# Performance work log

Measured on AMD Instinct MI355X. Metric: run time of the kernel, lower is better.

## Reference

```python
import jax, jax.numpy as jnp
import numpy as np

N, H, S, D = 2, 8, 2048, 64

def setup_inputs() -> dict:
    key = jax.random.key(0)
    k1, k2, k3, k4 = jax.random.split(key, 4)
    queries = jax.random.normal(k1, (N, H, S, D), dtype=jnp.float32)
    keys = jax.random.normal(k2, (N, H, S, D), dtype=jnp.float32)
    values = jax.random.normal(k3, (N, H, S, D), dtype=jnp.float32)
    attn_mask = jax.random.randint(k4, (1, 1, S, S), 0, 2, dtype=jnp.int32)
    return {"queries": queries, "keys": keys, "values": values, "attn_mask": attn_mask}

def reference(queries, keys, values, attn_mask):
    # Faithful to the torch code: softmax over axis=2 (query/seq axis) for Q,
    # softmax over axis=1 (heads axis) for K, exactly as written.
    Q = jax.nn.softmax(queries, axis=2)
    K = jax.nn.softmax(keys, axis=1)
    attention_weights = jnp.einsum('nhqd,nhkd->nhqk', Q, K)  # [N,H,S,S]
    attention_weights = jnp.where(attn_mask == 0, -jnp.inf, attention_weights)
    attention_weights = jax.nn.softmax(attention_weights, axis=-1)
    context = jnp.einsum('nhqk,nhkd->nhqd', attention_weights, values)
    return context, attention_weights
```

## Files before the change

### kernel.cpp

```cpp
#include <hip/hip_runtime.h>

#define S 2048
#define Dh 64
#define NH 16
#define SD (S*Dh)
#define SSZ ((size_t)S*(size_t)S)

typedef __attribute__((ext_vector_type(4))) float f32x4;
typedef __attribute__((ext_vector_type(8))) short s16x8;

#define WSB_QSUM 0
#define WSB_RINV 4096
#define WSB_MASK 135168
#define WSB_QS   659456
#define WSB_KS   (WSB_QS + 4194304)
#define WSB_VT   (WSB_KS + 4194304)

__device__ __forceinline__ ushort f2bf(float x) {
    unsigned u = __builtin_bit_cast(unsigned, x);
    u = (u + 0x7fffu + ((u >> 16) & 1u)) >> 16;
    return (ushort)u;
}

__device__ __forceinline__ void gload_lds16(const ushort* g, ushort* l) {
    __builtin_amdgcn_global_load_lds(
        (const __attribute__((address_space(1))) unsigned int*)(const void*)g,
        (__attribute__((address_space(3))) unsigned int*)(void*)l,
        16, 0, 0);
}

__global__ void k_qsum(const float* __restrict__ q, float* __restrict__ qsum) {
    const int head  = blockIdx.x >> 5;
    const int chunk = blockIdx.x & 31;
    const int t = threadIdx.x;
    const int d = t & 63, sg = t >> 6;
    const float* qh = q + (size_t)head * SD;
    const int s0 = chunk * 64;
    float acc = 0.f;
#pragma unroll
    for (int i = 0; i < 16; ++i) {
        int s = s0 + sg + 4 * i;
        acc += __expf(qh[s * Dh + d]);
    }
    __shared__ float part[4][64];
    part[sg][d] = acc;
    __syncthreads();
    if (sg == 0)
        atomicAdd(&qsum[head * 64 + d], part[0][d] + part[1][d] + part[2][d] + part[3][d]);
}

__global__ void k_qnorm(const float* __restrict__ q, const float* __restrict__ qsum,
                        ushort* __restrict__ Qs) {
    const int gid = blockIdx.x * 256 + threadIdx.x;
    const int i0 = gid * 8;
    const int head = i0 >> 17;
    const int d0 = i0 & 63;
    const float4 a = ((const float4*)(q + i0))[0];
    const float4 b = ((const float4*)(q + i0))[1];
    const float* qs = qsum + head * 64 + d0;
    s16x8 o;
    o[0] = (short)f2bf(__expf(a.x) / qs[0]);
    o[1] = (short)f2bf(__expf(a.y) / qs[1]);
    o[2] = (short)f2bf(__expf(a.z) / qs[2]);
    o[3] = (short)f2bf(__expf(a.w) / qs[3]);
    o[4] = (short)f2bf(__expf(b.x) / qs[4]);
    o[5] = (short)f2bf(__expf(b.y) / qs[5]);
    o[6] = (short)f2bf(__expf(b.z) / qs[6]);
    o[7] = (short)f2bf(__expf(b.w) / qs[7]);
    *(s16x8*)(Qs + i0) = o;
}

__global__ void k_ksoft(const float* __restrict__ kin, ushort* __restrict__ Ks) {
    const int gid = blockIdx.x * 256 + threadIdx.x;
    const int n = gid >> 17;
    const int rem = gid & (SD - 1);
    const float* base = kin + (size_t)n * 8 * SD + rem;
    float x[8];
    float sum = 0.f;
#pragma unroll
    for (int h = 0; h < 8; ++h) { x[h] = __expf(base[(size_t)h * SD]); sum += x[h]; }
    const float inv = 1.f / sum;
    ushort* ob = Ks + (size_t)n * 8 * SD + rem;
#pragma unroll
    for (int h = 0; h < 8; ++h) ob[(size_t)h * SD] = f2bf(x[h] * inv);
}

__global__ void k_vt(const float* __restrict__ V, ushort* __restrict__ Vt) {
    const int head = blockIdx.x >> 5, kt = blockIdx.x & 31;
    const int t = threadIdx.x;
    __shared__ float sv[64 * 68];
    const float4* src = (const float4*)(V + (size_t)head * SD + (size_t)kt * 64 * 64);
#pragma unroll
    for (int i = 0; i < 4; ++i) {
        int idx = t + 256 * i;
        int row = idx >> 4, c4 = idx & 15;
        *(float4*)&sv[row * 68 + c4 * 4] = src[idx];
    }
    __syncthreads();
    const int d = t >> 2, seg = t & 3;
    s16x8 v0, v1;
#pragma unroll
    for (int j = 0; j < 8; ++j) v0[j] = (short)f2bf(sv[(seg * 16 + j) * 68 + d]);
#pragma unroll
    for (int j = 0; j < 8; ++j) v1[j] = (short)f2bf(sv[(seg * 16 + 8 + j) * 68 + d]);
    ushort* dst = Vt + (size_t)head * SD + (size_t)d * S + kt * 64 + seg * 16;
    *(s16x8*)dst = v0;
    *(s16x8*)(dst + 8) = v1;
}

__global__ void k_mask(const int* __restrict__ mask, unsigned long long* __restrict__ bmt) {
    const int t = threadIdx.x;
    const int g = blockIdx.x * 4 + (t >> 6);
    const int lane = t & 63;
#pragma unroll
    for (int it = 0; it < 16; ++it) {
        int w = g * 16 + it;
        int m = mask[(size_t)w * 64 + lane];
        unsigned long long b = __ballot(m != 0);
        if (lane == 0) bmt[(size_t)(w & 31) * S + (w >> 5)] = b;
    }
}

__global__ __launch_bounds__(256, 4) void k_ctx(
        const ushort* __restrict__ Qs, const ushort* __restrict__ Ks,
        const ushort* __restrict__ Vt, const unsigned long long* __restrict__ bmt,
        float* __restrict__ ctx, float* __restrict__ rinv) {
    const int head = blockIdx.x, qt = blockIdx.y;
    const int q0 = qt * 32;
    const int t = threadIdx.x;
    const int lane = t & 63, w = t >> 6;
    const int wq = w & 1, kh = w >> 1;
    const int lm = lane & 15, lg = lane >> 4;
    const int q = q0 + 16 * wq + lm;

    __shared__ __align__(16) char smem[21760];
    ushort* sK = (ushort*)smem;
    ushort* sV = (ushort*)(smem + 8192);
    ushort* Pl = (ushort*)(smem + 16384);
    float*  redrs = (float*)(smem + 21504);
    float*  redo  = (float*)smem;

    const ushort* Qb = Qs + (size_t)head * SD;
    const ushort* Kb = Ks + (size_t)head * SD;
    const ushort* Vb = Vt + (size_t)head * SD;

    s16x8 bq[2];
#pragma unroll
    for (int h = 0; h < 2; ++h)
        bq[h] = *(const s16x8*)(Qb + (size_t)q * 64 + 32 * h + 8 * lg);

    f32x4 o[4];
#pragma unroll
    for (int dj = 0; dj < 4; ++dj) o[dj] = (f32x4){0.f, 0.f, 0.f, 0.f};
    float rs = 0.f;
    uint* prow = (uint*)&Pl[(w * 16 + lm) * 40];

    for (int kt = 0; kt < 32; ++kt) {
        const int k0 = kt * 64;
        __syncthreads();
#pragma unroll
        for (int i = 0; i < 2; ++i) {
            const int idx = t + 256 * i;
            const int row = idx >> 3, seg = idx & 7;
            const int sw = (seg ^ (row & 7)) * 8;
            gload_lds16(Kb + (size_t)(k0 + row) * 64 + sw, &sK[idx * 8]);
            gload_lds16(Vb + (size_t)row * S + k0 + sw, &sV[idx * 8]);
        }
        __syncthreads();

        f32x4 sc[2];
        sc[0] = (f32x4){0.f, 0.f, 0.f, 0.f};
        sc[1] = (f32x4){0.f, 0.f, 0.f, 0.f};
#pragma unroll
        for (int h = 0; h < 2; ++h)
#pragma unroll
            for (int jj = 0; jj < 2; ++jj) {
                const int row = 16 * (2 * kh + jj) + lm;
                s16x8 ak = *(const s16x8*)&sK[row * 64 + (((4 * h + lg) ^ (lm & 7)) * 8)];
                sc[jj] = __builtin_amdgcn_mfma_f32_16x16x32_bf16(ak, bq[h], sc[jj], 0, 0, 0);
            }
        const unsigned long long m64 = bmt[(size_t)kt * S + q];
        float rsum = 0.f;
#pragma unroll
        for (int jj = 0; jj < 2; ++jj)
#pragma unroll
            for (int p = 0; p < 2; ++p) {
                const int kloc = 16 * jj + 4 * lg + 2 * p;
                const int kbit = 32 * kh + kloc;
                const float e0 = ((m64 >> kbit) & 1ULL) ? __expf(sc[jj][2 * p]) : 0.f;
                const float e1 = ((m64 >> (kbit + 1)) & 1ULL) ? __expf(sc[jj][2 * p + 1]) : 0.f;
                rsum += e0 + e1;
                prow[kloc >> 1] = ((uint)f2bf(e1) << 16) | (uint)f2bf(e0);
            }
        rsum += __shfl_xor(rsum, 16);
        rsum += __shfl_xor(rsum, 32);
        rs += rsum;

        const s16x8 pb = *(const s16x8*)&Pl[(w * 16 + lm) * 40 + 8 * lg];
#pragma unroll
        for (int dj = 0; dj < 4; ++dj) {
            const int vrow = 16 * dj + lm;
            s16x8 av = *(const s16x8*)&sV[vrow * 64 + (((4 * kh + lg) ^ (lm & 7)) * 8)];
            o[dj] = __builtin_amdgcn_mfma_f32_16x16x32_bf16(av, pb, o[dj], 0, 0, 0);
        }
    }

    __syncthreads();
    if (kh == 1) {
        float* dst = redo + (wq * 64 + lane) * 20;
#pragma unroll
        for (int dj = 0; dj < 4; ++dj) *(f32x4*)&dst[dj * 4] = o[dj];
        if (lg == 0) redrs[wq * 16 + lm] = rs;
    }
    __syncthreads();
    if (kh == 0) {
        const float inv = 1.f / (rs + redrs[wq * 16 + lm]);
        if (lg == 0) rinv[head * S + q] = inv;
        const float* src = redo + (wq * 64 + lane) * 20;
        float* cb = ctx + (size_t)head * SD + (size_t)q * 64;
#pragma unroll
        for (int dj = 0; dj < 4; ++dj) {
            f32x4 oo = (o[dj] + *(const f32x4*)&src[dj * 4]) * inv;
            *(f32x4*)(cb + 16 * dj + 4 * lg) = oo;
        }
    }
}

__global__ __launch_bounds__(256, 4) void k_awrite(
        const ushort* __restrict__ Qs, const ushort* __restrict__ Ks,
        const unsigned long long* __restrict__ bmt, const float* __restrict__ rinv,
        float* __restrict__ A) {
    const int head = blockIdx.x, qt = blockIdx.y, kc = blockIdx.z;
    const int q0 = qt * 64;
    const int t = threadIdx.x;
    const int lane = t & 63, wv = t >> 6;
    const int lm = lane & 15, lg = lane >> 4;
    const int q = q0 + 16 * wv + lm;

    __shared__ __align__(16) char smem[33792];
    ushort* sK = (ushort*)smem;
    float* sP = (float*)(smem + 16384);

    const ushort* Qb = Qs + (size_t)head * SD;
    const ushort* Kb = Ks + (size_t)head * SD;
    float* Ah = A + (size_t)head * SSZ;

    auto stage = [&](int b, int k0) {
#pragma unroll
        for (int i = 0; i < 2; ++i) {
            const int idx = t + 256 * i;
            const int row = idx >> 3, seg = idx & 7;
            gload_lds16(Kb + (size_t)(k0 + row) * 64 + ((seg ^ (row & 7)) * 8),
                        &sK[b * 4096 + idx * 8]);
        }
    };

    s16x8 bq[2];
#pragma unroll
    for (int h = 0; h < 2; ++h)
        bq[h] = *(const s16x8*)(Qb + (size_t)q * 64 + 32 * h + 8 * lg);
    const float invr = rinv[head * S + q];
    float* sPw = &sP[wv * 16 * 68];

    stage(0, kc * 512);
    unsigned long long m64 = bmt[(size_t)(kc * 8) * S + q];
    __syncthreads();

    for (int kt8 = 0; kt8 < 8; ++kt8) {
        const int k0 = kc * 512 + kt8 * 64;
        const int cur = kt8 & 1;
        if (kt8 < 7) stage(cur ^ 1, k0 + 64);
        const unsigned long long m64n =
            (kt8 < 7) ? bmt[(size_t)((k0 >> 6) + 1) * S + q] : 0ULL;

        f32x4 sc[4];
#pragma unroll
        for (int j = 0; j < 4; ++j) sc[j] = (f32x4){0.f, 0.f, 0.f, 0.f};
#pragma unroll
        for (int h = 0; h < 2; ++h)
#pragma unroll
            for (int j = 0; j < 4; ++j) {
                s16x8 ak = *(const s16x8*)&sK[cur * 4096 + (16 * j + lm) * 64 +
                                              (((4 * h + lg) ^ (lm & 7)) * 8)];
                sc[j] = __builtin_amdgcn_mfma_f32_16x16x32_bf16(ak, bq[h], sc[j], 0, 0, 0);
            }

#pragma unroll
        for (int j = 0; j < 4; ++j) {
            f32x4 pv;
#pragma unroll
            for (int r = 0; r < 4; ++r) {
                const int b = 16 * j + 4 * lg + r;
                pv[r] = ((m64 >> b) & 1ULL) ? __expf(sc[j][r]) * invr : 0.f;
            }
            *(f32x4*)&sPw[lm * 68 + 16 * j + 4 * lg] = pv;
        }
#pragma unroll
        for (int pass = 0; pass < 4; ++pass) {
            const int rr = (lane >> 4) + 4 * pass;
            f32x4 pv = *(const f32x4*)&sPw[rr * 68 + (lane & 15) * 4];
            __builtin_nontemporal_store(pv,
                (f32x4*)&Ah[(size_t)(q0 + 16 * wv + rr) * S + k0 + (lane & 15) * 4]);
        }
        __syncthreads();
        m64 = m64n;
    }
}

extern "C" void kernel_launch(void* const* d_in, const int* in_sizes, int n_in,
                              void* d_out, int out_size, void* d_ws, size_t ws_size,
                              hipStream_t stream) {
    const float* q = (const float*)d_in[0];
    const float* k = (const float*)d_in[1];
    const float* v = (const float*)d_in[2];
    const int* mask = (const int*)d_in[3];
    float* out = (float*)d_out;
    char* ws = (char*)d_ws;

    float* qsum = (float*)(ws + WSB_QSUM);
    float* rinv = (float*)(ws + WSB_RINV);
    unsigned long long* bm = (unsigned long long*)(ws + WSB_MASK);
    ushort* Qs = (ushort*)(ws + WSB_QS);
    ushort* Ks = (ushort*)(ws + WSB_KS);
    ushort* Vt = (ushort*)(ws + WSB_VT);

    (void)hipMemsetAsync(d_ws, 0, 4096, stream);
    k_qsum<<<512, 256, 0, stream>>>(q, qsum);
    k_mask<<<1024, 256, 0, stream>>>(mask, bm);
    k_qnorm<<<1024, 256, 0, stream>>>(q, qsum, Qs);
    k_ksoft<<<1024, 256, 0, stream>>>(k, Ks);
    k_vt<<<512, 256, 0, stream>>>(v, Vt);
    k_ctx<<<dim3(16, 64), 256, 0, stream>>>(Qs, Ks, Vt, bm, out, rinv);
    k_awrite<<<dim3(16, 32, 4), 256, 0, stream>>>(Qs, Ks, bm, rinv, out + (size_t)NH * SD);
}
```

Baseline: 383.4 us.

## Switch k_ctx to 32x32x16 MFMA with 128-key tiles and 4-way key split

Rewrites the context kernel so each wave computes a 32x32 score tile with 32x32x16 bf16 MFMA over a 128-key tile, splitting keys across all four waves instead of 2 query x 2 key halves. The P matrix is rearranged in registers via cross-half lane shuffles rather than a round trip through LDS, and the final reduction sums four wave partials through shared memory. This halves the number of K/V tile loop iterations and barriers and removes LDS traffic for P, at the cost of more LDS (37.5KB vs 21.7KB), which may lower occupancy, and a heavier 4-way epilogue reduction.

After: 377.0 us. No clear change (-1.7%).

```diff
diff --git a/kernel.cpp b/kernel.cpp
--- a/kernel.cpp
+++ b/kernel.cpp
@@ -7,7 +7,9 @@
 #define SSZ ((size_t)S*(size_t)S)
 
 typedef __attribute__((ext_vector_type(4))) float f32x4;
+typedef __attribute__((ext_vector_type(16))) float f32x16;
 typedef __attribute__((ext_vector_type(8))) short s16x8;
+typedef __attribute__((ext_vector_type(4))) unsigned int u32x4;
 
 #define WSB_QSUM 0
 #define WSB_RINV 4096
@@ -129,100 +131,134 @@
     const int q0 = qt * 32;
     const int t = threadIdx.x;
     const int lane = t & 63, w = t >> 6;
-    const int wq = w & 1, kh = w >> 1;
-    const int lm = lane & 15, lg = lane >> 4;
-    const int q = q0 + 16 * wq + lm;
-
-    __shared__ __align__(16) char smem[21760];
+    const int ql = lane & 31, hi = lane >> 5;
+    const int q = q0 + ql;
+
+    __shared__ __align__(16) char smem[37504];
     ushort* sK = (ushort*)smem;
-    ushort* sV = (ushort*)(smem + 8192);
-    ushort* Pl = (ushort*)(smem + 16384);
-    float*  redrs = (float*)(smem + 21504);
-    float*  redo  = (float*)smem;
+    ushort* sV = (ushort*)(smem + 16384);
+    float* redo  = (float*)smem;
+    float* redrs = (float*)(smem + 36864);
+    float* sInv  = (float*)(smem + 37376);
 
     const ushort* Qb = Qs + (size_t)head * SD;
     const ushort* Kb = Ks + (size_t)head * SD;
     const ushort* Vb = Vt + (size_t)head * SD;
 
-    s16x8 bq[2];
-#pragma unroll
-    for (int h = 0; h < 2; ++h)
-        bq[h] = *(const s16x8*)(Qb + (size_t)q * 64 + 32 * h + 8 * lg);
-
-    f32x4 o[4];
-#pragma unroll
-    for (int dj = 0; dj < 4; ++dj) o[dj] = (f32x4){0.f, 0.f, 0.f, 0.f};
+    s16x8 bq[4];
+#pragma unroll
+    for (int s = 0; s < 4; ++s)
+        bq[s] = *(const s16x8*)(Qb + (size_t)q * 64 + 16 * s + 8 * hi);
+
+    f32x16 o0, o1;
+#pragma unroll
+    for (int r = 0; r < 16; ++r) { o0[r] = 0.f; o1[r] = 0.f; }
     float rs = 0.f;
-    uint* prow = (uint*)&Pl[(w * 16 + lm) * 40];
-
-    for (int kt = 0; kt < 32; ++kt) {
-        const int k0 = kt * 64;
+
+    for (int mt = 0; mt < 16; ++mt) {
+        const int k0 = mt * 128;
         __syncthreads();
 #pragma unroll
-        for (int i = 0; i < 2; ++i) {
+        for (int i = 0; i < 4; ++i) {
             const int idx = t + 256 * i;
-            const int row = idx >> 3, seg = idx & 7;
-            const int sw = (seg ^ (row & 7)) * 8;
-            gload_lds16(Kb + (size_t)(k0 + row) * 64 + sw, &sK[idx * 8]);
-            gload_lds16(Vb + (size_t)row * S + k0 + sw, &sV[idx * 8]);
+            const int row = idx >> 3, c = idx & 7;
+            gload_lds16(Kb + (size_t)(k0 + row) * 64 + ((c ^ (row & 7)) * 8), &sK[idx * 8]);
+        }
+#pragma unroll
+        for (int i = 0; i < 4; ++i) {
+            const int idx = t + 256 * i;
+            const int row = idx >> 4, c = idx & 15;
+            gload_lds16(Vb + (size_t)row * S + k0 + ((c ^ (row & 7)) * 8), &sV[idx * 8]);
         }
         __syncthreads();
 
-        f32x4 sc[2];
-        sc[0] = (f32x4){0.f, 0.f, 0.f, 0.f};
-        sc[1] = (f32x4){0.f, 0.f, 0.f, 0.f};
-#pragma unroll
-        for (int h = 0; h < 2; ++h)
-#pragma unroll
-            for (int jj = 0; jj < 2; ++jj) {
-                const int row = 16 * (2 * kh + jj) + lm;
-                s16x8 ak = *(const s16x8*)&sK[row * 64 + (((4 * h + lg) ^ (lm & 7)) * 8)];
-                sc[jj] = __builtin_amdgcn_mfma_f32_16x16x32_bf16(ak, bq[h], sc[jj], 0, 0, 0);
-            }
-        const unsigned long long m64 = bmt[(size_t)kt * S + q];
+        f32x16 sc;
+#pragma unroll
+        for (int r = 0; r < 16; ++r) sc[r] = 0.f;
+        const int arow = 32 * w + ql;
+#pragma unroll
+        for (int s = 0; s < 4; ++s) {
+            const s16x8 ak = *(const s16x8*)&sK[arow * 64 + (((2 * s + hi) ^ (arow & 7)) * 8)];
+            sc = __builtin_amdgcn_mfma_f32_32x32x16_bf16(ak, bq[s], sc, 0, 0, 0);
+        }
+
+        const unsigned long long m64 = bmt[(size_t)(2 * mt + (w >> 1)) * S + q];
+        const unsigned mbits = (w & 1) ? (unsigned)(m64 >> 32) : (unsigned)m64;
+
+        unsigned pk8[8];
         float rsum = 0.f;
 #pragma unroll
-        for (int jj = 0; jj < 2; ++jj)
-#pragma unroll
-            for (int p = 0; p < 2; ++p) {
-                const int kloc = 16 * jj + 4 * lg + 2 * p;
-                const int kbit = 32 * kh + kloc;
-                const float e0 = ((m64 >> kbit) & 1ULL) ? __expf(sc[jj][2 * p]) : 0.f;
-                const float e1 = ((m64 >> (kbit + 1)) & 1ULL) ? __expf(sc[jj][2 * p + 1]) : 0.f;
-                rsum += e0 + e1;
-                prow[kloc >> 1] = ((uint)f2bf(e1) << 16) | (uint)f2bf(e0);
-            }
-        rsum += __shfl_xor(rsum, 16);
+        for (int g = 0; g < 8; ++g) {
+            const int r0 = 2 * g;
+            const int kb = (r0 & 3) + 8 * (r0 >> 2) + 4 * hi;
+            const float e0 = ((mbits >> kb) & 1u) ? __expf(sc[r0]) : 0.f;
+            const float e1 = ((mbits >> (kb + 1)) & 1u) ? __expf(sc[r0 + 1]) : 0.f;
+            rsum += e0 + e1;
+            pk8[g] = ((unsigned)f2bf(e1) << 16) | (unsigned)f2bf(e0);
+        }
         rsum += __shfl_xor(rsum, 32);
         rs += rsum;
 
-        const s16x8 pb = *(const s16x8*)&Pl[(w * 16 + lm) * 40 + 8 * lg];
-#pragma unroll
-        for (int dj = 0; dj < 4; ++dj) {
-            const int vrow = 16 * dj + lm;
-            s16x8 av = *(const s16x8*)&sV[vrow * 64 + (((4 * kh + lg) ^ (lm & 7)) * 8)];
-            o[dj] = __builtin_amdgcn_mfma_f32_16x16x32_bf16(av, pb, o[dj], 0, 0, 0);
-        }
-    }
-
-    __syncthreads();
-    if (kh == 1) {
-        float* dst = redo + (wq * 64 + lane) * 20;
-#pragma unroll
-        for (int dj = 0; dj < 4; ++dj) *(f32x4*)&dst[dj * 4] = o[dj];
-        if (lg == 0) redrs[wq * 16 + lm] = rs;
-    }
-    __syncthreads();
-    if (kh == 0) {
-        const float inv = 1.f / (rs + redrs[wq * 16 + lm]);
-        if (lg == 0) rinv[head * S + q] = inv;
-        const float* src = redo + (wq * 64 + lane) * 20;
-        float* cb = ctx + (size_t)head * SD + (size_t)q * 64;
-#pragma unroll
-        for (int dj = 0; dj < 4; ++dj) {
-            f32x4 oo = (o[dj] + *(const f32x4*)&src[dj * 4]) * inv;
-            *(f32x4*)(cb + 16 * dj + 4 * lg) = oo;
-        }
+        const unsigned x1 = __shfl_xor(hi ? pk8[0] : pk8[2], 32);
+        const unsigned x2 = __shfl_xor(hi ? pk8[1] : pk8[3], 32);
+        const unsigned x3 = __shfl_xor(hi ? pk8[4] : pk8[6], 32);
+        const unsigned x4 = __shfl_xor(hi ? pk8[5] : pk8[7], 32);
+        const u32x4 w0 = hi ? (u32x4){x1, x2, pk8[2], pk8[3]}
+                            : (u32x4){pk8[0], pk8[1], x1, x2};
+        const u32x4 w1 = hi ? (u32x4){x3, x4, pk8[6], pk8[7]}
+                            : (u32x4){pk8[4], pk8[5], x3, x4};
+        const s16x8 pb0 = __builtin_bit_cast(s16x8, w0);
+        const s16x8 pb1 = __builtin_bit_cast(s16x8, w1);
+
+#pragma unroll
+        for (int cs = 0; cs < 2; ++cs) {
+            const s16x8 pbv = cs ? pb1 : pb0;
+            {
+                const int vrow = ql;
+                const int ch = (4 * w + 2 * cs + hi) ^ (vrow & 7);
+                const s16x8 av = *(const s16x8*)&sV[vrow * 128 + ch * 8];
+                o0 = __builtin_amdgcn_mfma_f32_32x32x16_bf16(av, pbv, o0, 0, 0, 0);
+            }
+            {
+                const int vrow = 32 + ql;
+                const int ch = (4 * w + 2 * cs + hi) ^ (vrow & 7);
+                const s16x8 av = *(const s16x8*)&sV[vrow * 128 + ch * 8];
+                o1 = __builtin_amdgcn_mfma_f32_32x32x16_bf16(av, pbv, o1, 0, 0, 0);
+            }
+        }
+    }
+
+    __syncthreads();
+    {
+        float* dst = &redo[(w * 64 + lane) * 36];
+#pragma unroll
+        for (int g = 0; g < 4; ++g)
+            *(f32x4*)&dst[4 * g] = (f32x4){o0[4*g], o0[4*g+1], o0[4*g+2], o0[4*g+3]};
+#pragma unroll
+        for (int g = 0; g < 4; ++g)
+            *(f32x4*)&dst[16 + 4 * g] = (f32x4){o1[4*g], o1[4*g+1], o1[4*g+2], o1[4*g+3]};
+        if (hi == 0) redrs[w * 32 + ql] = rs;
+    }
+    __syncthreads();
+    if (t < 32) {
+        const float inv = 1.f / (redrs[t] + redrs[32 + t] + redrs[64 + t] + redrs[96 + t]);
+        rinv[head * S + q0 + t] = inv;
+        sInv[t] = inv;
+    }
+    __syncthreads();
+#pragma unroll
+    for (int cc = 0; cc < 2; ++cc) {
+        const int c = t + 256 * cc;
+        const int l = c & 63, rq = c >> 6;
+        f32x4 sum = *(const f32x4*)&redo[l * 36 + rq * 4];
+#pragma unroll
+        for (int ww = 1; ww < 4; ++ww)
+            sum += *(const f32x4*)&redo[(ww * 64 + l) * 36 + rq * 4];
+        const int qc = l & 31, hc = l >> 5;
+        const int dtc = rq >> 2, rg = rq & 3;
+        const int d0 = 32 * dtc + 4 * hc + 8 * rg;
+        sum *= sInv[qc];
+        *(f32x4*)(ctx + (size_t)head * SD + (size_t)(q0 + qc) * 64 + d0) = sum;
     }
 }
 
```
